# Kernel tuning notes

Measured on AMD Instinct MI355X. Metric: run time of the kernel, lower is better.

The kernel has to match this reference:

```python
import jax, jax.numpy as jnp
import numpy as np

NUM_HEADS = 16

def setup_inputs() -> dict:
    key = jax.random.key(0)
    ks = jax.random.split(key, 5)
    E = 1024
    x = jax.random.normal(ks[0], (2, 2048, E), dtype=jnp.float32)
    w_in = jax.random.normal(ks[1], (3 * E, E), dtype=jnp.float32) * (E ** -0.5)
    b_in = jax.random.normal(ks[2], (3 * E,), dtype=jnp.float32) * 0.02
    w_out = jax.random.normal(ks[3], (E, E), dtype=jnp.float32) * (E ** -0.5)
    b_out = jax.random.normal(ks[4], (E,), dtype=jnp.float32) * 0.02
    return {"x": x, "w_in": w_in, "b_in": b_in, "w_out": w_out, "b_out": b_out}


def reference(x, w_in, b_in, w_out, b_out):
    B, N, E = x.shape
    H = NUM_HEADS
    Dh = E // H
    # fused QKV projection (torch Linear: x @ W^T + b)
    qkv = x @ w_in.T + b_in                      # [B, N, 3E]
    q, k, v = jnp.split(qkv, 3, axis=-1)
    # [B, H, N, Dh]
    q = q.reshape(B, N, H, Dh).transpose(0, 2, 1, 3)
    k = k.reshape(B, N, H, Dh).transpose(0, 2, 1, 3)
    v = v.reshape(B, N, H, Dh).transpose(0, 2, 1, 3)
    scale = Dh ** -0.5
    scores = jnp.einsum("bhqd,bhkd->bhqk", q, k) * scale  # [B, H, N, N]
    attn = jax.nn.softmax(scores, axis=-1)
    out = jnp.einsum("bhqk,bhkd->bhqd", attn, v)          # [B, H, N, Dh]
    out = out.transpose(0, 2, 1, 3).reshape(B, N, E)
    return out @ w_out.T + b_out
```

## Files before the change

### kernel.cpp

```cpp
#include <hip/hip_runtime.h>


typedef __bf16 bf16;
typedef __bf16 bf16x8 __attribute__((ext_vector_type(8)));
typedef __bf16 bf16x4 __attribute__((ext_vector_type(4)));
typedef float  f32x4  __attribute__((ext_vector_type(4)));

#define MFMA16(a, b, c) __builtin_amdgcn_mfma_f32_16x16x32_bf16((a), (b), (c), 0, 0, 0)

#define SC2 0.18033688011112042f

__device__ __forceinline__ void gld_lds16(const void* g, void* l) {
  __builtin_amdgcn_global_load_lds((const __attribute__((address_space(1))) void*)g,
                                   (__attribute__((address_space(3))) void*)l,
                                   16, 0, 0);
}

__device__ __forceinline__ float exp2_raw(float x) {
  float r;
  asm("v_exp_f32 %0, %1" : "=v"(r) : "v"(x));
  return r;
}

__global__ __launch_bounds__(256) void cast3_kernel(
    const float* __restrict__ x, const float* __restrict__ wi,
    const float* __restrict__ wo, bf16* __restrict__ xb,
    bf16* __restrict__ wib, bf16* __restrict__ wob) {
  const int i = (blockIdx.x * 256 + threadIdx.x) * 4;
  const float* s; bf16* d; int off;
  if (i < 4194304)      { s = x;  d = xb;  off = i; }
  else if (i < 7340032) { s = wi; d = wib; off = i - 4194304; }
  else                  { s = wo; d = wob; off = i - 7340032; }
  const float4 v = *(const float4*)(s + off);
  bf16x4 o;
  o[0] = (bf16)v.x; o[1] = (bf16)v.y; o[2] = (bf16)v.z; o[3] = (bf16)v.w;
  *(bf16x4*)(d + off) = o;
}

__global__ __launch_bounds__(256) void gemm_qkv_kernel(
    const bf16* __restrict__ A,
    const bf16* __restrict__ B,
    const float* __restrict__ bias,
    bf16* __restrict__ qb, bf16* __restrict__ kb, bf16* __restrict__ vb) {
  constexpr int K = 1024;
  __shared__ __align__(16) char smem[128 * 136 * 2];
  bf16* As = (bf16*)smem;
  bf16* Bs = (bf16*)(smem + 8192);
  const int tid  = threadIdx.x;
  const int lane = tid & 63;
  const int wave = tid >> 6;
  const int m0 = blockIdx.y * 128;
  const int n0 = blockIdx.x * 128;
  const int r_ = tid >> 2;
  const int k_ = (tid & 3) * 8;
  const int lr = lane & 15, lg = lane >> 4;
  const int wm = (wave >> 1) * 64, wn = (wave & 1) * 64;

  f32x4 acc[4][4];
#pragma unroll
  for (int i = 0; i < 4; ++i)
#pragma unroll
    for (int j = 0; j < 4; ++j) acc[i][j] = (f32x4){0.f, 0.f, 0.f, 0.f};

  for (int k0 = 0; k0 < K; k0 += 32) {
    __syncthreads();
    gld_lds16(A + (size_t)(m0 + r_) * K + k0 + k_,      (char*)As + tid * 16);
    gld_lds16(A + (size_t)(m0 + 64 + r_) * K + k0 + k_, (char*)As + 4096 + tid * 16);
    gld_lds16(B + (size_t)(n0 + r_) * K + k0 + k_,      (char*)Bs + tid * 16);
    gld_lds16(B + (size_t)(n0 + 64 + r_) * K + k0 + k_, (char*)Bs + 4096 + tid * 16);
    __syncthreads();

    bf16x8 af[4], bfr[4];
#pragma unroll
    for (int i = 0; i < 4; ++i)
      af[i] = *(const bf16x8*)((const char*)As + (size_t)((wm + i * 16 + lr) * 32 + lg * 8) * 2);
#pragma unroll
    for (int j = 0; j < 4; ++j)
      bfr[j] = *(const bf16x8*)((const char*)Bs + (size_t)((wn + j * 16 + lr) * 32 + lg * 8) * 2);
#pragma unroll
    for (int i = 0; i < 4; ++i)
#pragma unroll
      for (int j = 0; j < 4; ++j) acc[i][j] = MFMA16(af[i], bfr[j], acc[i][j]);
  }

  __syncthreads();
  bf16* T = (bf16*)smem;
  const int which = n0 >> 10;
  const int wi0 = n0 & 1023;
  const int bb = m0 >> 11, nn0 = m0 & 2047;

  if (which < 2) {
    const float scl = (which == 0) ? SC2 : 1.0f;
#pragma unroll
    for (int j = 0; j < 4; ++j) {
      const int tcol = wn + j * 16 + lr;
      const float bv = bias[n0 + tcol];
#pragma unroll
      for (int i = 0; i < 4; ++i)
#pragma unroll
        for (int r = 0; r < 4; ++r) {
          const int trow = wm + i * 16 + lg * 4 + r;
          T[trow * 136 + tcol] = (bf16)((acc[i][j][r] + bv) * scl);
        }
    }
    __syncthreads();
    bf16* dst = (which == 0) ? qb : kb;
    const int l = tid & 15, g = tid >> 4;
    const int cc = l * 8;
    const int h = (wi0 + cc) >> 6, d = cc & 63;
#pragma unroll
    for (int p = 0; p < 8; ++p) {
      const int rr = p * 16 + g;
      *(bf16x8*)(dst + ((size_t)(bb * 16 + h) * 2048 + nn0 + rr) * 64 + d) =
          *(const bf16x8*)(T + rr * 136 + cc);
    }
  } else {
#pragma unroll
    for (int j = 0; j < 4; ++j) {
      const int c = wn + j * 16 + lr;
      const float bv = bias[n0 + c];
#pragma unroll
      for (int i = 0; i < 4; ++i)
#pragma unroll
        for (int r = 0; r < 4; ++r) {
          const int rr = wm + i * 16 + lg * 4 + r;
          T[c * 136 + rr] = (bf16)(acc[i][j][r] + bv);
        }
    }
    __syncthreads();
    const int l = tid & 15, g = tid >> 4;
    const int nof = l * 8;
#pragma unroll
    for (int p = 0; p < 8; ++p) {
      const int c = p * 16 + g;
      const int h = (wi0 + c) >> 6, d = (wi0 + c) & 63;
      *(bf16x8*)(vb + ((size_t)(bb * 16 + h) * 64 + d) * 2048 + nn0 + nof) =
          *(const bf16x8*)(T + c * 136 + nof);
    }
  }
}

__global__ __launch_bounds__(256) void flash_attn_kernel(
    const bf16* __restrict__ q, const bf16* __restrict__ k,
    const bf16* __restrict__ vt, bf16* __restrict__ o) {
  __shared__ bf16 Ks[2][64 * 64];
  __shared__ bf16 Vs[2][64 * 64];
  __shared__ bf16 Pl[4][2][16 * 64];

  const int tid  = threadIdx.x;
  const int lane = tid & 63;
  const int wave = tid >> 6;
  const int lr = lane & 15, lg = lane >> 4;
  const int qt = blockIdx.x;
  const int bh = blockIdx.y;
  const bf16* qp = q  + (size_t)bh * (2048 * 64);
  const bf16* kp = k  + (size_t)bh * (2048 * 64);
  const bf16* vp = vt + (size_t)bh * (64 * 2048);
  const int q0 = qt * 128 + wave * 32;
  const int wmask = (lr & 7) << 4;

  int srow[2], scol[2];
#pragma unroll
  for (int p = 0; p < 2; ++p) {
    const int L = p * 4096 + tid * 16;
    srow[p] = L >> 7;
    scol[p] = ((L & 127) ^ ((srow[p] & 7) << 4)) >> 1;
  }

  bf16x8 qf[2][2];
#pragma unroll
  for (int qi = 0; qi < 2; ++qi)
#pragma unroll
    for (int t = 0; t < 2; ++t)
      qf[qi][t] = *(const bf16x8*)(qp + (size_t)(q0 + qi * 16 + lr) * 64 + t * 32 + lg * 8);

  bf16x8 ones;
#pragma unroll
  for (int i = 0; i < 8; ++i) ones[i] = (bf16)1.0f;

  f32x4 oacc[2][4];
#pragma unroll
  for (int qi = 0; qi < 2; ++qi)
#pragma unroll
    for (int j = 0; j < 4; ++j) oacc[qi][j] = (f32x4){0.f, 0.f, 0.f, 0.f};
  f32x4 lacc[2];
#pragma unroll
  for (int qi = 0; qi < 2; ++qi) lacc[qi] = (f32x4){0.f, 0.f, 0.f, 0.f};

#pragma unroll
  for (int p = 0; p < 2; ++p) {
    const int L = p * 4096 + tid * 16;
    gld_lds16(kp + (size_t)srow[p] * 64 + scol[p],       (char*)Ks[0] + L);
    gld_lds16(vp + (size_t)srow[p] * 2048 + 0 + scol[p], (char*)Vs[0] + L);
  }
  __syncthreads();

  int buf = 0;
  for (int t = 0; t < 32; ++t) {
    if (t + 1 < 32) {
      const int nkv = t * 64 + 64;
#pragma unroll
      for (int p = 0; p < 2; ++p) {
        const int L = p * 4096 + tid * 16;
        gld_lds16(kp + (size_t)(nkv + srow[p]) * 64 + scol[p], (char*)Ks[buf ^ 1] + L);
        gld_lds16(vp + (size_t)srow[p] * 2048 + nkv + scol[p], (char*)Vs[buf ^ 1] + L);
      }
    }

    f32x4 s[2][4];
#pragma unroll
    for (int qi = 0; qi < 2; ++qi)
#pragma unroll
      for (int sub = 0; sub < 4; ++sub) s[qi][sub] = (f32x4){0.f, 0.f, 0.f, 0.f};
    __builtin_amdgcn_s_setprio(1);
#pragma unroll
    for (int sub = 0; sub < 4; ++sub) {
#pragma unroll
      for (int tt = 0; tt < 2; ++tt) {
        const int row = sub * 16 + lr;
        const int byte = (row << 7) + (((tt * 32 + lg * 8) << 1) ^ ((row & 7) << 4));
        bf16x8 kf = *(const bf16x8*)((const char*)Ks[buf] + byte);
#pragma unroll
        for (int qi = 0; qi < 2; ++qi) s[qi][sub] = MFMA16(kf, qf[qi][tt], s[qi][sub]);
      }
    }
    __builtin_amdgcn_s_setprio(0);

#pragma unroll
    for (int qi = 0; qi < 2; ++qi) {
      char* pl = (char*)&Pl[wave][qi][0] + lr * 128;
#pragma unroll
      for (int sub = 0; sub < 4; ++sub) {
        const float e0 = exp2_raw(s[qi][sub][0]);
        const float e1 = exp2_raw(s[qi][sub][1]);
        const float e2 = exp2_raw(s[qi][sub][2]);
        const float e3 = exp2_raw(s[qi][sub][3]);
        unsigned p01, p23;
        asm("v_cvt_pk_bf16_f32 %0, %1, %2" : "=v"(p01) : "v"(e0), "v"(e1));
        asm("v_cvt_pk_bf16_f32 %0, %1, %2" : "=v"(p23) : "v"(e2), "v"(e3));
        uint2 w; w.x = p01; w.y = p23;
        *(uint2*)(pl + ((sub * 32 + lg * 8) ^ wmask)) = w;
      }
    }
    bf16x8 pa[2][2];
#pragma unroll
    for (int qi = 0; qi < 2; ++qi)
#pragma unroll
      for (int kk = 0; kk < 2; ++kk)
        pa[qi][kk] = *(const bf16x8*)((const char*)&Pl[wave][qi][0] + lr * 128 +
                                      ((kk * 64 + lg * 16) ^ wmask));

    __builtin_amdgcn_s_setprio(1);
#pragma unroll
    for (int j = 0; j < 4; ++j) {
#pragma unroll
      for (int kk = 0; kk < 2; ++kk) {
        const int row = j * 16 + lr;
        const int byte = (row << 7) + (((kk * 32 + lg * 8) << 1) ^ ((row & 7) << 4));
        bf16x8 vf = *(const bf16x8*)((const char*)Vs[buf] + byte);
#pragma unroll
        for (int qi = 0; qi < 2; ++qi) oacc[qi][j] = MFMA16(pa[qi][kk], vf, oacc[qi][j]);
      }
    }
#pragma unroll
    for (int qi = 0; qi < 2; ++qi)
#pragma unroll
      for (int kk = 0; kk < 2; ++kk)
        lacc[qi] = MFMA16(pa[qi][kk], ones, lacc[qi]);
    __builtin_amdgcn_s_setprio(0);

    __syncthreads();
    buf ^= 1;
  }

  const int b = bh >> 4, h = bh & 15;
#pragma unroll
  for (int qi = 0; qi < 2; ++qi) {
    float inv[4];
#pragma unroll
    for (int r = 0; r < 4; ++r) inv[r] = 1.f / lacc[qi][r];
#pragma unroll
    for (int j = 0; j < 4; ++j) {
#pragma unroll
      for (int r = 0; r < 4; ++r) {
        const int qrow = q0 + qi * 16 + lg * 4 + r;
        o[((size_t)(b * 2048 + qrow)) * 1024 + h * 64 + j * 16 + lr] =
            (bf16)(oacc[qi][j][r] * inv[r]);
      }
    }
  }
}

__global__ __launch_bounds__(256) void gemm_out_kernel(
    const bf16* __restrict__ A,
    const bf16* __restrict__ B,
    const float* __restrict__ bias,
    float* __restrict__ out) {
  constexpr int K = 1024;
  __shared__ bf16 As[128 * 32];
  __shared__ bf16 Bs[128 * 32];
  const int tid  = threadIdx.x;
  const int lane = tid & 63;
  const int wave = tid >> 6;
  const int m0 = blockIdx.y * 128;
  const int n0 = blockIdx.x * 128;
  const int r_ = tid >> 2;
  const int k_ = (tid & 3) * 8;
  const int lr = lane & 15, lg = lane >> 4;
  const int wm = (wave >> 1) * 64, wn = (wave & 1) * 64;

  f32x4 acc[4][4];
#pragma unroll
  for (int i = 0; i < 4; ++i)
#pragma unroll
    for (int j = 0; j < 4; ++j) acc[i][j] = (f32x4){0.f, 0.f, 0.f, 0.f};

  for (int k0 = 0; k0 < K; k0 += 32) {
    __syncthreads();
    gld_lds16(A + (size_t)(m0 + r_) * K + k0 + k_,      (char*)As + tid * 16);
    gld_lds16(A + (size_t)(m0 + 64 + r_) * K + k0 + k_, (char*)As + 4096 + tid * 16);
    gld_lds16(B + (size_t)(n0 + r_) * K + k0 + k_,      (char*)Bs + tid * 16);
    gld_lds16(B + (size_t)(n0 + 64 + r_) * K + k0 + k_, (char*)Bs + 4096 + tid * 16);
    __syncthreads();

    bf16x8 af[4], bfr[4];
#pragma unroll
    for (int i = 0; i < 4; ++i)
      af[i] = *(const bf16x8*)((const char*)As + (size_t)((wm + i * 16 + lr) * 32 + lg * 8) * 2);
#pragma unroll
    for (int j = 0; j < 4; ++j)
      bfr[j] = *(const bf16x8*)((const char*)Bs + (size_t)((wn + j * 16 + lr) * 32 + lg * 8) * 2);
#pragma unroll
    for (int i = 0; i < 4; ++i)
#pragma unroll
      for (int j = 0; j < 4; ++j) acc[i][j] = MFMA16(af[i], bfr[j], acc[i][j]);
  }

#pragma unroll
  for (int j = 0; j < 4; ++j) {
    const int col = n0 + wn + j * 16 + lr;
    const float bv = bias[col];
#pragma unroll
    for (int i = 0; i < 4; ++i) {
#pragma unroll
      for (int r = 0; r < 4; ++r) {
        const int row = m0 + wm + i * 16 + lg * 4 + r;
        out[(size_t)row * 1024 + col] = acc[i][j][r] + bv;
      }
    }
  }
}

extern "C" void kernel_launch(void* const* d_in, const int* in_sizes, int n_in,
                              void* d_out, int out_size, void* d_ws, size_t ws_size,
                              hipStream_t stream) {
  const float* x     = (const float*)d_in[0];
  const float* w_in  = (const float*)d_in[1];
  const float* b_in  = (const float*)d_in[2];
  const float* w_out = (const float*)d_in[3];
  const float* b_out = (const float*)d_in[4];
  float* out = (float*)d_out;

  char* ws = (char*)d_ws;
  const size_t MB = 1ull << 20;
  bf16* xb  = (bf16*)(ws + 0 * MB);
  bf16* wib = (bf16*)(ws + 8 * MB);
  bf16* wob = (bf16*)(ws + 14 * MB);
  bf16* qb  = (bf16*)(ws + 16 * MB);
  bf16* kb  = (bf16*)(ws + 24 * MB);
  bf16* vb  = (bf16*)(ws + 32 * MB);
  bf16* ab  = (bf16*)(ws + 40 * MB);

  cast3_kernel<<<dim3(8192), dim3(256), 0, stream>>>(x, w_in, w_out, xb, wib, wob);
  gemm_qkv_kernel<<<dim3(24, 32), dim3(256), 0, stream>>>(xb, wib, b_in, qb, kb, vb);
  flash_attn_kernel<<<dim3(16, 32), dim3(256), 0, stream>>>(qb, kb, vb, ab);
  gemm_out_kernel<<<dim3(8, 32), dim3(256), 0, stream>>>(ab, wob, b_out, out);
}
```

Baseline: 204.9 us.

## Use 8 waves per attention block with 16 query rows each and XCD-aware block mapping

The flash attention kernel now launches 512-thread blocks of 8 waves, and each wave handles 16 query rows instead of 32. Each thread loads one K and one V chunk per tile instead of two. Blocks are remapped from a 1-D grid so that all query tiles of a given head land on the same XCD, which improves L2 reuse of K/V. This cuts per-wave register use and raises wave-level parallelism, but each K/V fragment read from LDS now feeds only one MFMA instead of two, lowering LDS reuse.

```diff
diff --git a/kernel.cpp b/kernel.cpp
--- a/kernel.cpp
+++ b/kernel.cpp
@@ -140,78 +140,60 @@
   }
 }
 
-__global__ __launch_bounds__(256) void flash_attn_kernel(
+__global__ __launch_bounds__(512) void flash_attn_kernel(
     const bf16* __restrict__ q, const bf16* __restrict__ k,
     const bf16* __restrict__ vt, bf16* __restrict__ o) {
   __shared__ bf16 Ks[2][64 * 64];
   __shared__ bf16 Vs[2][64 * 64];
-  __shared__ bf16 Pl[4][2][16 * 64];
+  __shared__ bf16 Pl[8][16 * 64];
 
   const int tid  = threadIdx.x;
   const int lane = tid & 63;
   const int wave = tid >> 6;
   const int lr = lane & 15, lg = lane >> 4;
-  const int qt = blockIdx.x;
-  const int bh = blockIdx.y;
+  const int id   = blockIdx.x;
+  const int slot = id >> 3;
+  const int bh   = (id & 7) * 4 + (slot >> 4);
+  const int qt   = slot & 15;
   const bf16* qp = q  + (size_t)bh * (2048 * 64);
   const bf16* kp = k  + (size_t)bh * (2048 * 64);
   const bf16* vp = vt + (size_t)bh * (64 * 2048);
-  const int q0 = qt * 128 + wave * 32;
+  const int q0 = qt * 128 + wave * 16;
   const int wmask = (lr & 7) << 4;
 
-  int srow[2], scol[2];
-#pragma unroll
-  for (int p = 0; p < 2; ++p) {
-    const int L = p * 4096 + tid * 16;
-    srow[p] = L >> 7;
-    scol[p] = ((L & 127) ^ ((srow[p] & 7) << 4)) >> 1;
-  }
-
-  bf16x8 qf[2][2];
-#pragma unroll
-  for (int qi = 0; qi < 2; ++qi)
-#pragma unroll
-    for (int t = 0; t < 2; ++t)
-      qf[qi][t] = *(const bf16x8*)(qp + (size_t)(q0 + qi * 16 + lr) * 64 + t * 32 + lg * 8);
+  const int L = tid * 16;
+  const int srow = L >> 7;
+  const int scol = ((L & 127) ^ ((srow & 7) << 4)) >> 1;
+
+  bf16x8 qf[2];
+#pragma unroll
+  for (int t = 0; t < 2; ++t)
+    qf[t] = *(const bf16x8*)(qp + (size_t)(q0 + lr) * 64 + t * 32 + lg * 8);
 
   bf16x8 ones;
 #pragma unroll
   for (int i = 0; i < 8; ++i) ones[i] = (bf16)1.0f;
 
-  f32x4 oacc[2][4];
-#pragma unroll
-  for (int qi = 0; qi < 2; ++qi)
-#pragma unroll
-    for (int j = 0; j < 4; ++j) oacc[qi][j] = (f32x4){0.f, 0.f, 0.f, 0.f};
-  f32x4 lacc[2];
-#pragma unroll
-  for (int qi = 0; qi < 2; ++qi) lacc[qi] = (f32x4){0.f, 0.f, 0.f, 0.f};
-
-#pragma unroll
-  for (int p = 0; p < 2; ++p) {
-    const int L = p * 4096 + tid * 16;
-    gld_lds16(kp + (size_t)srow[p] * 64 + scol[p],       (char*)Ks[0] + L);
-    gld_lds16(vp + (size_t)srow[p] * 2048 + 0 + scol[p], (char*)Vs[0] + L);
-  }
+  f32x4 oacc[4];
+#pragma unroll
+  for (int j = 0; j < 4; ++j) oacc[j] = (f32x4){0.f, 0.f, 0.f, 0.f};
+  f32x4 lacc = (f32x4){0.f, 0.f, 0.f, 0.f};
+
+  gld_lds16(kp + (size_t)srow * 64 + scol,       (char*)Ks[0] + L);
+  gld_lds16(vp + (size_t)srow * 2048 + 0 + scol, (char*)Vs[0] + L);
   __syncthreads();
 
   int buf = 0;
   for (int t = 0; t < 32; ++t) {
     if (t + 1 < 32) {
       const int nkv = t * 64 + 64;
-#pragma unroll
-      for (int p = 0; p < 2; ++p) {
-        const int L = p * 4096 + tid * 16;
-        gld_lds16(kp + (size_t)(nkv + srow[p]) * 64 + scol[p], (char*)Ks[buf ^ 1] + L);
-        gld_lds16(vp + (size_t)srow[p] * 2048 + nkv + scol[p], (char*)Vs[buf ^ 1] + L);
-      }
-    }
-
-    f32x4 s[2][4];
-#pragma unroll
-    for (int qi = 0; qi < 2; ++qi)
-#pragma unroll
-      for (int sub = 0; sub < 4; ++sub) s[qi][sub] = (f32x4){0.f, 0.f, 0.f, 0.f};
+      gld_lds16(kp + (size_t)(nkv + srow) * 64 + scol, (char*)Ks[buf ^ 1] + L);
+      gld_lds16(vp + (size_t)srow * 2048 + nkv + scol, (char*)Vs[buf ^ 1] + L);
+    }
+
+    f32x4 s[4];
+#pragma unroll
+    for (int sub = 0; sub < 4; ++sub) s[sub] = (f32x4){0.f, 0.f, 0.f, 0.f};
     __builtin_amdgcn_s_setprio(1);
 #pragma unroll
     for (int sub = 0; sub < 4; ++sub) {
@@ -220,21 +202,19 @@
         const int row = sub * 16 + lr;
         const int byte = (row << 7) + (((tt * 32 + lg * 8) << 1) ^ ((row & 7) << 4));
         bf16x8 kf = *(const bf16x8*)((const char*)Ks[buf] + byte);
-#pragma unroll
-        for (int qi = 0; qi < 2; ++qi) s[qi][sub] = MFMA16(kf, qf[qi][tt], s[qi][sub]);
+        s[sub] = MFMA16(kf, qf[tt], s[sub]);
       }
     }
     __builtin_amdgcn_s_setprio(0);
 
-#pragma unroll
-    for (int qi = 0; qi < 2; ++qi) {
-      char* pl = (char*)&Pl[wave][qi][0] + lr * 128;
+    {
+      char* pl = (char*)&Pl[wave][0] + lr * 128;
 #pragma unroll
       for (int sub = 0; sub < 4; ++sub) {
-        const float e0 = exp2_raw(s[qi][sub][0]);
-        const float e1 = exp2_raw(s[qi][sub][1]);
-        const float e2 = exp2_raw(s[qi][sub][2]);
-        const float e3 = exp2_raw(s[qi][sub][3]);
+        const float e0 = exp2_raw(s[sub][0]);
+        const float e1 = exp2_raw(s[sub][1]);
+        const float e2 = exp2_raw(s[sub][2]);
+        const float e3 = exp2_raw(s[sub][3]);
         unsigned p01, p23;
         asm("v_cvt_pk_bf16_f32 %0, %1, %2" : "=v"(p01) : "v"(e0), "v"(e1));
         asm("v_cvt_pk_bf16_f32 %0, %1, %2" : "=v"(p23) : "v"(e2), "v"(e3));
@@ -242,13 +222,11 @@
         *(uint2*)(pl + ((sub * 32 + lg * 8) ^ wmask)) = w;
       }
     }
-    bf16x8 pa[2][2];
-#pragma unroll
-    for (int qi = 0; qi < 2; ++qi)
-#pragma unroll
-      for (int kk = 0; kk < 2; ++kk)
-        pa[qi][kk] = *(const bf16x8*)((const char*)&Pl[wave][qi][0] + lr * 128 +
-                                      ((kk * 64 + lg * 16) ^ wmask));
+    bf16x8 pa[2];
+#pragma unroll
+    for (int kk = 0; kk < 2; ++kk)
+      pa[kk] = *(const bf16x8*)((const char*)&Pl[wave][0] + lr * 128 +
+                                ((kk * 64 + lg * 16) ^ wmask));
 
     __builtin_amdgcn_s_setprio(1);
 #pragma unroll
@@ -258,15 +236,11 @@
         const int row = j * 16 + lr;
         const int byte = (row << 7) + (((kk * 32 + lg * 8) << 1) ^ ((row & 7) << 4));
         bf16x8 vf = *(const bf16x8*)((const char*)Vs[buf] + byte);
-#pragma unroll
-        for (int qi = 0; qi < 2; ++qi) oacc[qi][j] = MFMA16(pa[qi][kk], vf, oacc[qi][j]);
+        oacc[j] = MFMA16(pa[kk], vf, oacc[j]);
       }
     }
 #pragma unroll
-    for (int qi = 0; qi < 2; ++qi)
-#pragma unroll
-      for (int kk = 0; kk < 2; ++kk)
-        lacc[qi] = MFMA16(pa[qi][kk], ones, lacc[qi]);
+    for (int kk = 0; kk < 2; ++kk) lacc = MFMA16(pa[kk], ones, lacc);
     __builtin_amdgcn_s_setprio(0);
 
     __syncthreads();
@@ -274,19 +248,16 @@
   }
 
   const int b = bh >> 4, h = bh & 15;
-#pragma unroll
-  for (int qi = 0; qi < 2; ++qi) {
-    float inv[4];
-#pragma unroll
-    for (int r = 0; r < 4; ++r) inv[r] = 1.f / lacc[qi][r];
-#pragma unroll
-    for (int j = 0; j < 4; ++j) {
-#pragma unroll
-      for (int r = 0; r < 4; ++r) {
-        const int qrow = q0 + qi * 16 + lg * 4 + r;
-        o[((size_t)(b * 2048 + qrow)) * 1024 + h * 64 + j * 16 + lr] =
-            (bf16)(oacc[qi][j][r] * inv[r]);
-      }
+  float inv[4];
+#pragma unroll
+  for (int r = 0; r < 4; ++r) inv[r] = 1.f / lacc[r];
+#pragma unroll
+  for (int j = 0; j < 4; ++j) {
+#pragma unroll
+    for (int r = 0; r < 4; ++r) {
+      const int qrow = q0 + lg * 4 + r;
+      o[((size_t)(b * 2048 + qrow)) * 1024 + h * 64 + j * 16 + lr] =
+          (bf16)(oacc[j][r] * inv[r]);
     }
   }
 }
@@ -373,6 +344,6 @@
 
   cast3_kernel<<<dim3(8192), dim3(256), 0, stream>>>(x, w_in, w_out, xb, wib, wob);
   gemm_qkv_kernel<<<dim3(24, 32), dim3(256), 0, stream>>>(xb, wib, b_in, qb, kb, vb);
-  flash_attn_kernel<<<dim3(16, 32), dim3(256), 0, stream>>>(qb, kb, vb, ab);
+  flash_attn_kernel<<<dim3(512), dim3(512), 0, stream>>>(qb, kb, vb, ab);
   gemm_out_kernel<<<dim3(8, 32), dim3(256), 0, stream>>>(ab, wob, b_out, out);
 }
```

Result: faster. 195.1 us (-4.8%).
